# Optimization experiments

Measured on AMD Instinct MI355X. Metric: run time of the kernel, lower is better.

The kernel has to match this reference:

```python
import jax, jax.numpy as jnp
import numpy as np

N_SRC = 500000   # rows per source matrix
D = 64           # columns
L = 400000       # rows gathered per source
N_OUT = 3 * L    # total output rows (1.2M)


def setup_inputs() -> dict:
    key = jax.random.key(0)
    k = jax.random.split(key, 8)
    mat0 = jax.random.normal(k[0], (N_SRC, D), dtype=jnp.float32)
    mat1 = jax.random.normal(k[1], (N_SRC, D), dtype=jnp.float32)
    mat2 = jax.random.normal(k[2], (N_SRC, D), dtype=jnp.float32)
    from0 = jax.random.randint(k[3], (L,), 0, N_SRC, dtype=jnp.int32)
    from1 = jax.random.randint(k[4], (L,), 0, N_SRC, dtype=jnp.int32)
    from2 = jax.random.randint(k[5], (L,), 0, N_SRC, dtype=jnp.int32)
    # idx_tos: disjoint partition of output rows (every out row written once)
    perm = jax.random.permutation(k[6], N_OUT)
    to0, to1, to2 = perm[:L], perm[L:2 * L], perm[2 * L:]
    return {"mat0": mat0, "mat1": mat1, "mat2": mat2,
            "from0": from0, "from1": from1, "from2": from2,
            "to0": to0, "to1": to1, "to2": to2}


def reference(mat0, mat1, mat2, from0, from1, from2, to0, to1, to2):
    # out[x_to] = mat[x_from] for each (mat, x_from, x_to) triple
    num_rows = to0.shape[0] + to1.shape[0] + to2.shape[0]
    out = jnp.zeros((num_rows, mat0.shape[1]), dtype=mat0.dtype)
    out = out.at[to0].set(mat0[from0])
    out = out.at[to1].set(mat1[from1])
    out = out.at[to2].set(mat2[from2])
    return out
```

## Files before the change

kernel.cpp:

```cpp
#include <hip/hip_runtime.h>


#define L_ROWS 400000
#define VEC_PER_ROW 16

__global__ __launch_bounds__(256) void multi_index_select_kernel(
    const float4* __restrict__ mat0,
    const float4* __restrict__ mat1,
    const float4* __restrict__ mat2,
    const int*    __restrict__ from0,
    const int*    __restrict__ from1,
    const int*    __restrict__ from2,
    const int*    __restrict__ to0,
    const int*    __restrict__ to1,
    const int*    __restrict__ to2,
    float4*       __restrict__ out)
{
    long long tid = (long long)blockIdx.x * blockDim.x + threadIdx.x;
    int row = (int)(tid >> 4);
    int col = (int)(tid & 15);
    if (row >= 3 * L_ROWS) return;

    const float4* mat;
    const int* from;
    const int* to;
    int r;
    if (row < L_ROWS) {
        mat = mat0; from = from0; to = to0; r = row;
    } else if (row < 2 * L_ROWS) {
        mat = mat1; from = from1; to = to1; r = row - L_ROWS;
    } else {
        mat = mat2; from = from2; to = to2; r = row - 2 * L_ROWS;
    }

    int src = from[r];
    int dst = to[r];

    out[(size_t)dst * VEC_PER_ROW + col] = mat[(size_t)src * VEC_PER_ROW + col];
}

extern "C" void kernel_launch(void* const* d_in, const int* in_sizes, int n_in,
                              void* d_out, int out_size, void* d_ws, size_t ws_size,
                              hipStream_t stream) {
    const float4* mat0 = (const float4*)d_in[0];
    const float4* mat1 = (const float4*)d_in[1];
    const float4* mat2 = (const float4*)d_in[2];
    const int* from0 = (const int*)d_in[3];
    const int* from1 = (const int*)d_in[4];
    const int* from2 = (const int*)d_in[5];
    const int* to0   = (const int*)d_in[6];
    const int* to1   = (const int*)d_in[7];
    const int* to2   = (const int*)d_in[8];
    float4* out = (float4*)d_out;

    const long long total_threads = (long long)3 * L_ROWS * VEC_PER_ROW;
    const int block = 256;
    const int grid = (int)((total_threads + block - 1) / block);

    multi_index_select_kernel<<<grid, block, 0, stream>>>(
        mat0, mat1, mat2, from0, from1, from2, to0, to1, to2, out);
}
```

Baseline: 535.6 us.

## Invert scatter into per-output code table and gather with sequential writes

Adds a pre-pass that builds a per-output-row code (source matrix id packed with source row) in the workspace. A second kernel walks output rows in order, gathers from the chosen matrix and writes rows contiguously with nontemporal stores, four rows per thread. This replaces random-row writes with sequential ones, at the cost of an extra launch and a scattered 4-byte code write per row. It relies on the destination indices covering every output row exactly once and on source indices fitting in 19 bits; when the workspace is too small it falls back to the old kernel.

After: 553.4 us. 3.3% more time.

```diff
diff --git a/kernel.cpp b/kernel.cpp
--- a/kernel.cpp
+++ b/kernel.cpp
@@ -2,7 +2,64 @@
 
 
 #define L_ROWS 400000
+#define N_OUT (3 * L_ROWS)
 #define VEC_PER_ROW 16
+#define CH (N_OUT / 4)
+#define K_SHIFT 19
+#define SRC_MASK ((1u << K_SHIFT) - 1u)
+
+typedef float nfloat4 __attribute__((ext_vector_type(4)));
+
+__global__ __launch_bounds__(256) void build_codes_kernel(
+    const int* __restrict__ from0,
+    const int* __restrict__ from1,
+    const int* __restrict__ from2,
+    const int* __restrict__ to0,
+    const int* __restrict__ to1,
+    const int* __restrict__ to2,
+    unsigned int* __restrict__ code)
+{
+    int i = blockIdx.x * blockDim.x + threadIdx.x;
+    if (i >= L_ROWS) return;
+    code[to0[i]] = (unsigned int)from0[i];
+    code[to1[i]] = (unsigned int)from1[i] | (1u << K_SHIFT);
+    code[to2[i]] = (unsigned int)from2[i] | (2u << K_SHIFT);
+}
+
+__global__ __launch_bounds__(256) void gather_seq_write_kernel(
+    const nfloat4* __restrict__ mat0,
+    const nfloat4* __restrict__ mat1,
+    const nfloat4* __restrict__ mat2,
+    const unsigned int* __restrict__ code,
+    nfloat4* __restrict__ out)
+{
+    int tid = blockIdx.x * blockDim.x + threadIdx.x;
+    int col = tid & 15;
+    int rid = tid >> 4;
+    if (rid >= CH) return;
+
+    unsigned int c0 = code[rid];
+    unsigned int c1 = code[rid + CH];
+    unsigned int c2 = code[rid + 2 * CH];
+    unsigned int c3 = code[rid + 3 * CH];
+
+    unsigned int k0 = c0 >> K_SHIFT, k1 = c1 >> K_SHIFT;
+    unsigned int k2 = c2 >> K_SHIFT, k3 = c3 >> K_SHIFT;
+    const nfloat4* p0 = (k0 == 0) ? mat0 : ((k0 == 1) ? mat1 : mat2);
+    const nfloat4* p1 = (k1 == 0) ? mat0 : ((k1 == 1) ? mat1 : mat2);
+    const nfloat4* p2 = (k2 == 0) ? mat0 : ((k2 == 1) ? mat1 : mat2);
+    const nfloat4* p3 = (k3 == 0) ? mat0 : ((k3 == 1) ? mat1 : mat2);
+
+    nfloat4 v0 = p0[(size_t)(c0 & SRC_MASK) * VEC_PER_ROW + col];
+    nfloat4 v1 = p1[(size_t)(c1 & SRC_MASK) * VEC_PER_ROW + col];
+    nfloat4 v2 = p2[(size_t)(c2 & SRC_MASK) * VEC_PER_ROW + col];
+    nfloat4 v3 = p3[(size_t)(c3 & SRC_MASK) * VEC_PER_ROW + col];
+
+    __builtin_nontemporal_store(v0, &out[(size_t)rid * VEC_PER_ROW + col]);
+    __builtin_nontemporal_store(v1, &out[(size_t)(rid + CH) * VEC_PER_ROW + col]);
+    __builtin_nontemporal_store(v2, &out[(size_t)(rid + 2 * CH) * VEC_PER_ROW + col]);
+    __builtin_nontemporal_store(v3, &out[(size_t)(rid + 3 * CH) * VEC_PER_ROW + col]);
+}
 
 __global__ __launch_bounds__(256) void multi_index_select_kernel(
     const float4* __restrict__ mat0,
@@ -19,7 +76,7 @@
     long long tid = (long long)blockIdx.x * blockDim.x + threadIdx.x;
     int row = (int)(tid >> 4);
     int col = (int)(tid & 15);
-    if (row >= 3 * L_ROWS) return;
+    if (row >= N_OUT) return;
 
     const float4* mat;
     const int* from;
@@ -35,7 +92,6 @@
 
     int src = from[r];
     int dst = to[r];
-
     out[(size_t)dst * VEC_PER_ROW + col] = mat[(size_t)src * VEC_PER_ROW + col];
 }
 
@@ -53,10 +109,23 @@
     const int* to2   = (const int*)d_in[8];
     float4* out = (float4*)d_out;
 
-    const long long total_threads = (long long)3 * L_ROWS * VEC_PER_ROW;
-    const int block = 256;
-    const int grid = (int)((total_threads + block - 1) / block);
+    const size_t code_bytes = (size_t)N_OUT * sizeof(unsigned int);
 
-    multi_index_select_kernel<<<grid, block, 0, stream>>>(
-        mat0, mat1, mat2, from0, from1, from2, to0, to1, to2, out);
+    if (ws_size >= code_bytes) {
+        unsigned int* code = (unsigned int*)d_ws;
+
+        build_codes_kernel<<<(L_ROWS + 255) / 256, 256, 0, stream>>>(
+            from0, from1, from2, to0, to1, to2, code);
+
+        const int threads2 = CH * VEC_PER_ROW;
+        gather_seq_write_kernel<<<threads2 / 256, 256, 0, stream>>>(
+            (const nfloat4*)mat0, (const nfloat4*)mat1, (const nfloat4*)mat2,
+            code, (nfloat4*)out);
+    } else {
+        const long long total_threads = (long long)N_OUT * VEC_PER_ROW;
+        const int block = 256;
+        const int grid = (int)((total_threads + block - 1) / block);
+        multi_index_select_kernel<<<grid, block, 0, stream>>>(
+            mat0, mat1, mat2, from0, from1, from2, to0, to1, to2, out);
+    }
 }
```
